# Performance work log

Hardware: AMD Instinct MI355X
Metric: run time of the kernel (lower is better)

## Reference

```python
import jax, jax.numpy as jnp
import numpy as np

EMBED_DIM = 768
NUM_HEADS = 12
HEAD_DIM = EMBED_DIM // NUM_HEADS


def setup_inputs() -> dict:
    key = jax.random.key(0)
    ks = jax.random.split(key, 5)
    B, N, D = 8, 1024, EMBED_DIM
    s = 1.0 / np.sqrt(D)
    x = jax.random.normal(ks[0], (B, N, D), dtype=jnp.float32)
    W_qkv = jax.random.normal(ks[1], (D, 3 * D), dtype=jnp.float32) * s
    b_qkv = jnp.zeros((3 * D,), dtype=jnp.float32)
    W_proj = jax.random.normal(ks[2], (D, D), dtype=jnp.float32) * s
    b_proj = jnp.zeros((D,), dtype=jnp.float32)
    return {"x": x, "W_qkv": W_qkv, "b_qkv": b_qkv, "W_proj": W_proj, "b_proj": b_proj}


def reference(x, W_qkv, b_qkv, W_proj, b_proj):
    B, N, D = x.shape
    H, Hd = NUM_HEADS, HEAD_DIM
    scale = Hd ** -0.5
    qkv = x @ W_qkv + b_qkv                      # (B, N, 3D)
    qkv = qkv.reshape(B, N, 3, H, Hd).transpose(2, 0, 3, 1, 4)  # (3, B, H, N, Hd)
    q, k, v = qkv[0], qkv[1], qkv[2]
    attn = jnp.einsum('bhnd,bhmd->bhnm', q, k) * scale  # (B, H, N, N)
    attn = jax.nn.softmax(attn, axis=-1)
    out = jnp.einsum('bhnm,bhmd->bhnd', attn, v)        # (B, H, N, Hd)
    out = out.transpose(0, 2, 1, 3).reshape(B, N, D)
    return out @ W_proj + b_proj
```

## Files before the change

kernel.cpp:

```cpp
#include <hip/hip_runtime.h>


#define B_   8
#define N_   1024
#define D_   768
#define H_   12
#define HD_  64

typedef __attribute__((ext_vector_type(4))) float f32x4;
typedef __attribute__((ext_vector_type(8))) short bf16x8;

__device__ __forceinline__ unsigned short f2bf(float f) {
    unsigned int u = __float_as_uint(f);
    u += 0x7fff + ((u >> 16) & 1);
    return (unsigned short)(u >> 16);
}
__device__ __forceinline__ unsigned int pk2(float a, float b) {
    return (unsigned int)f2bf(a) | ((unsigned int)f2bf(b) << 16);
}
__device__ __forceinline__ unsigned int pk2t(float a, float b) {
    return __builtin_amdgcn_perm(__float_as_uint(b), __float_as_uint(a), 0x07060302u);
}
__device__ __forceinline__ float truncbf(float f) {
    return __uint_as_float(__float_as_uint(f) & 0xFFFF0000u);
}
__device__ __forceinline__ void gl_lds16(const void* g, void* l) {
    __builtin_amdgcn_global_load_lds(
        (const __attribute__((address_space(1))) unsigned int*)g,
        (__attribute__((address_space(3))) unsigned int*)l, 16, 0, 0);
}
#define MFMA(a, b, c) __builtin_amdgcn_mfma_f32_16x16x32_bf16(a, b, c, 0, 0, 0)
#define BAR() do { __asm__ volatile("" ::: "memory"); \
    __builtin_amdgcn_s_barrier(); \
    __asm__ volatile("" ::: "memory"); } while (0)
#define WAITVM(n) do { __asm__ volatile("" ::: "memory"); \
    __builtin_amdgcn_s_waitcnt(0xF70 | (n)); \
    __asm__ volatile("" ::: "memory"); } while (0)
#define WAITLGKM() __asm__ volatile("s_waitcnt lgkmcnt(0)" ::: "memory")

__global__ __launch_bounds__(256) void prep_kernel(
    const float* __restrict__ x, const float* __restrict__ wqkv,
    const float* __restrict__ wproj,
    unsigned short* __restrict__ XB, unsigned short* __restrict__ WQT,
    unsigned short* __restrict__ WPT)
{
    const int bid = blockIdx.x;
    const int tid = threadIdx.x;
    if (bid < 3072) {
        int id = bid * 256 + tid;
        int r  = id & 127;
        int kc = (id >> 7) & 7;
        int ks = (id >> 10) % 12;
        int nt = id / 12288;
        const float* src = x + (size_t)(nt * 128 + r) * 768 + ks * 64 + kc * 8;
        float4 f0 = *(const float4*)src;
        float4 f1 = *(const float4*)(src + 4);
        uint4 o;
        o.x = pk2(f0.x, f0.y); o.y = pk2(f0.z, f0.w);
        o.z = pk2(f1.x, f1.y); o.w = pk2(f1.z, f1.w);
        *(uint4*)&XB[(size_t)id * 8] = o;
    } else if (bid < 3936) {
        int id = (bid - 3072) * 256 + tid;
        int fr = id & 127;
        int kc = (id >> 7) & 7;
        int ks = (id >> 10) % 12;
        int mt = id / 12288;
        float v[8];
#pragma unroll
        for (int j = 0; j < 8; ++j)
            v[j] = wqkv[(size_t)(ks * 64 + kc * 8 + j) * 2304 + mt * 128 + fr];
        uint4 o;
        o.x = pk2(v[0], v[1]); o.y = pk2(v[2], v[3]);
        o.z = pk2(v[4], v[5]); o.w = pk2(v[6], v[7]);
        *(uint4*)&WQT[(size_t)id * 8] = o;
    } else {
        int id = (bid - 3936) * 256 + tid;
        int fr = id & 63;
        int kc = (id >> 6) & 7;
        int ks = (id >> 9) % 12;
        int nt = id / 6144;
        float v[8];
#pragma unroll
        for (int j = 0; j < 8; ++j)
            v[j] = wproj[(size_t)(ks * 64 + kc * 8 + j) * 768 + nt * 64 + fr];
        uint4 o;
        o.x = pk2(v[0], v[1]); o.y = pk2(v[2], v[3]);
        o.z = pk2(v[4], v[5]); o.w = pk2(v[6], v[7]);
        *(uint4*)&WPT[(size_t)id * 8] = o;
    }
}

__global__ __launch_bounds__(256, 4) void qkv_gemm(
    const unsigned short* __restrict__ XB,
    const unsigned short* __restrict__ WQT,
    const float* __restrict__ bias,
    unsigned short* __restrict__ QS,
    unsigned short* __restrict__ KS,
    unsigned short* __restrict__ VS)
{
    __shared__ __align__(16) unsigned short sm[16384];

    const int tid = threadIdx.x;
    const int w = tid >> 6, lane = tid & 63;
    const int l15 = lane & 15, quad = lane >> 4;
    const int mt = blockIdx.x >> 6;
    const int nt = blockIdx.x & 63;
    const int m0w = (w & 1) * 64, n0w = (w >> 1) * 64;
    const float CS = 0.18033688f;

    char* smb = (char*)sm;
    const char* baseA = (const char*)(WQT + (size_t)(mt * 12) * 8192);
    const char* baseB = (const char*)(XB  + (size_t)(nt * 12) * 8192);

    auto issue = [&](int ks) {
        const char* sA = baseA + ks * 8192;
        const char* sB = baseB + ks * 8192;
        const int pb = ks & 1;
#pragma unroll
        for (int i = 0; i < 2; ++i) {
            const int c = w * 2 + i;
            gl_lds16(sA + (c * 64 + lane) * 16, smb + pb * 8192 + c * 1024);
            gl_lds16(sB + (c * 64 + lane) * 16, smb + 16384 + pb * 8192 + c * 1024);
        }
    };

    f32x4 acc[4][4];
    const f32x4 z = {0.f, 0.f, 0.f, 0.f};
#pragma unroll
    for (int t = 0; t < 4; ++t)
#pragma unroll
        for (int u = 0; u < 4; ++u) acc[t][u] = z;

    issue(0);
    for (int ks = 0; ks < 24; ++ks) {
        BAR();
        if (ks < 23) { issue(ks + 1); WAITVM(4); } else { WAITVM(0); }
        BAR();
        const unsigned short* Ab = sm + (ks & 1) * 4096;
        const unsigned short* Bb = sm + 8192 + (ks & 1) * 4096;
        bf16x8 af[4], bfv[4];
#pragma unroll
        for (int t = 0; t < 4; ++t)
            af[t] = *(const bf16x8*)(Ab + (quad * 128 + m0w + t * 16 + l15) * 8);
#pragma unroll
        for (int u = 0; u < 4; ++u)
            bfv[u] = *(const bf16x8*)(Bb + (quad * 128 + n0w + u * 16 + l15) * 8);
#pragma unroll
        for (int t = 0; t < 4; ++t)
#pragma unroll
            for (int u = 0; u < 4; ++u)
                acc[t][u] = MFMA(af[t], bfv[u], acc[t][u]);
    }

    const int part = mt / 6;
    BAR();

#pragma unroll
    for (int t = 0; t < 4; ++t) {
        int d = m0w + t * 16 + quad * 4;
        float4 bv = *(const float4*)&bias[part * 768 + (mt % 6) * 128 + d];
#pragma unroll
        for (int u = 0; u < 4; ++u) {
            int tok = n0w + u * 16 + l15;
            f32x4 a = acc[t][u];
            float v0 = a[0] + bv.x, v1 = a[1] + bv.y;
            float v2 = a[2] + bv.z, v3 = a[3] + bv.w;
            if (part == 0) { v0 *= CS; v1 *= CS; v2 *= CS; v3 *= CS; }
            if (part < 2) {
                unsigned off = tok * 256 + (((unsigned)(d * 2)) ^ ((tok & 7) << 4));
                uint2 pp; pp.x = pk2(v0, v1); pp.y = pk2(v2, v3);
                *(uint2*)(smb + off) = pp;
            } else {
                float vv[4] = {v0, v1, v2, v3};
#pragma unroll
                for (int r4 = 0; r4 < 4; ++r4) {
                    int dd = d + r4;
                    unsigned off = dd * 256 + (((unsigned)(tok * 2)) ^ ((dd & 7) << 4));
                    *(unsigned short*)(smb + off) = f2bf(vv[r4]);
                }
            }
        }
    }
    BAR();

    const int b = nt >> 3, qtc = nt & 7;
    if (part == 0) {
#pragma unroll
        for (int round = 0; round < 8; ++round) {
            int r = tid & 127;
            int kc = (tid >> 7) + round * 2;
            uint4 val = *(const uint4*)(smb + r * 256 +
                        (((unsigned)(kc << 4)) ^ ((r & 7) << 4)));
            int h = (mt % 6) * 2 + (kc >> 3);
            int bh = b * H_ + h;
            *(uint4*)(QS + (((size_t)(bh * 8 + qtc) * 1024) + (kc & 7) * 128 + r) * 8) = val;
        }
    } else if (part == 1) {
#pragma unroll
        for (int round = 0; round < 8; ++round) {
            int r = tid & 127;
            int kc = (tid >> 7) + round * 2;
            uint4 val = *(const uint4*)(smb + r * 256 +
                        (((unsigned)(kc << 4)) ^ ((r & 7) << 4)));
            int h = (mt % 6) * 2 + (kc >> 3);
            int bh = b * H_ + h;
            int kt = (qtc << 1) | (r >> 6);
            *(uint4*)(KS + (((size_t)(bh * 16 + kt) * 512) + (kc & 7) * 64 + (r & 63)) * 8) = val;
        }
    } else {
#pragma unroll
        for (int round = 0; round < 8; ++round) {
            int dd = tid & 127;
            int tc = (tid >> 7) + round * 2;
            uint4 val = *(const uint4*)(smb + dd * 256 +
                        (((unsigned)(tc << 4)) ^ ((dd & 7) << 4)));
            int h = (mt % 6) * 2 + (dd >> 6);
            int bh = b * H_ + h;
            int kt = (qtc << 1) | (tc >> 3);
            *(uint4*)(VS + (((size_t)(bh * 16 + kt) * 512) + (tc & 7) * 64 + (dd & 63)) * 8) = val;
        }
    }
}

__global__ __launch_bounds__(256, 3) void attn_kernel(
    const unsigned short* __restrict__ QS,
    const unsigned short* __restrict__ KS,
    const unsigned short* __restrict__ VS,
    unsigned short* __restrict__ AWS)
{
    __shared__ __align__(16) unsigned short sm[24576];

    const int tid = threadIdx.x;
    const int w = tid >> 6, lane = tid & 63;
    const int l15 = lane & 15, quad = lane >> 4;
    const int bh = blockIdx.x % 96;
    const int qt = blockIdx.x / 96;

    char* smb = (char*)sm;
    const char* kbase = (const char*)(KS + (size_t)(bh * 16) * 4096);
    const char* vbase = (const char*)(VS + (size_t)(bh * 16) * 4096);

    auto issue_tile = [&](int kt) {
        const char* ks_ = kbase + kt * 8192;
        const char* vs_ = vbase + kt * 8192;
        const int pb = kt & 1;
#pragma unroll
        for (int i = 0; i < 2; ++i) {
            const int c = w * 2 + i;
            gl_lds16(ks_ + (c * 64 + lane) * 16, smb + 16384 + pb * 8192 + c * 1024);
            gl_lds16(vs_ + (c * 64 + lane) * 16, smb + 32768 + pb * 8192 + c * 1024);
        }
    };

    const char* qslab = (const char*)(QS + (size_t)(bh * 8 + qt) * 8192);
#pragma unroll
    for (int i = 0; i < 4; ++i) {
        const int c = w * 4 + i;
        gl_lds16(qslab + (c * 64 + lane) * 16, smb + c * 1024);
    }
    issue_tile(0);

    WAITVM(4);
    BAR();
    bf16x8 qf[2][2];
#pragma unroll
    for (int u = 0; u < 2; ++u)
#pragma unroll
        for (int s = 0; s < 2; ++s)
            qf[u][s] = *(const bf16x8*)(sm + ((s * 4 + quad) * 128 + w * 32 + u * 16 + l15) * 8);
    WAITLGKM();
    BAR();

    f32x4 o[4][2];
    const f32x4 z = {0.f, 0.f, 0.f, 0.f};
#pragma unroll
    for (int t = 0; t < 4; ++t) { o[t][0] = z; o[t][1] = z; }
    float lsum[2] = {0.f, 0.f};

    char* pscr = smb + w * 4096;

    for (int kt = 0; kt < 16; ++kt) {
        BAR();
        if (kt < 15) { issue_tile(kt + 1); WAITVM(4); } else { WAITVM(0); }
        BAR();
        const unsigned short* Kb = sm + 8192 + (kt & 1) * 4096;
        const unsigned short* Vb = sm + 16384 + (kt & 1) * 4096;

        f32x4 s[4][2];
#pragma unroll
        for (int t = 0; t < 4; ++t) { s[t][0] = z; s[t][1] = z; }
#pragma unroll
        for (int ss = 0; ss < 2; ++ss) {
            bf16x8 kf[4];
#pragma unroll
            for (int t = 0; t < 4; ++t)
                kf[t] = *(const bf16x8*)(Kb + ((ss * 4 + quad) * 64 + t * 16 + l15) * 8);
#pragma unroll
            for (int t = 0; t < 4; ++t)
#pragma unroll
                for (int u = 0; u < 2; ++u)
                    s[t][u] = MFMA(kf[t], qf[u][ss], s[t][u]);
        }

#pragma unroll
        for (int u = 0; u < 2; ++u) {
#pragma unroll
            for (int t = 0; t < 4; ++t) {
                float p0 = truncbf(__builtin_amdgcn_exp2f(s[t][u][0]));
                float p1 = truncbf(__builtin_amdgcn_exp2f(s[t][u][1]));
                float p2 = truncbf(__builtin_amdgcn_exp2f(s[t][u][2]));
                float p3 = truncbf(__builtin_amdgcn_exp2f(s[t][u][3]));
                lsum[u] += (p0 + p1) + (p2 + p3);
                uint2 pw; pw.x = pk2t(p0, p1); pw.y = pk2t(p2, p3);
                *(uint2*)(pscr + u * 2048 + l15 * 128 +
                          ((t ^ (l15 & 3)) << 5) + quad * 8) = pw;
            }
        }
        WAITLGKM();

#pragma unroll
        for (int ss = 0; ss < 2; ++ss) {
            bf16x8 vf[4];
#pragma unroll
            for (int t = 0; t < 4; ++t)
                vf[t] = *(const bf16x8*)(Vb + ((ss * 4 + quad) * 64 + t * 16 + l15) * 8);
#pragma unroll
            for (int u = 0; u < 2; ++u) {
                bf16x8 pf = *(const bf16x8*)(pscr + u * 2048 + l15 * 128 +
                            (((2 * ss + (quad >> 1)) ^ (l15 & 3)) << 5) + (quad & 1) * 16);
#pragma unroll
                for (int t = 0; t < 4; ++t)
                    o[t][u] = MFMA(vf[t], pf, o[t][u]);
            }
        }
    }

    float inv[2];
#pragma unroll
    for (int u = 0; u < 2; ++u) {
        float l = lsum[u];
        l += __shfl_xor(l, 16, 64);
        l += __shfl_xor(l, 32, 64);
        inv[u] = 1.f / l;
    }

    BAR();
    char* tb = smb + 16384;
#pragma unroll
    for (int t = 0; t < 4; ++t) {
        int d = t * 16 + quad * 4;
#pragma unroll
        for (int u = 0; u < 2; ++u) {
            int q = w * 32 + u * 16 + l15;
            uint2 pp;
            pp.x = pk2(o[t][u][0] * inv[u], o[t][u][1] * inv[u]);
            pp.y = pk2(o[t][u][2] * inv[u], o[t][u][3] * inv[u]);
            unsigned off = q * 128 + (((unsigned)(d * 2)) ^ ((q & 7) << 4));
            *(uint2*)(tb + off) = pp;
        }
    }
    BAR();
    const int b = bh / H_, h = bh % H_;
    const int mtA = b * 8 + qt;
#pragma unroll
    for (int round = 0; round < 4; ++round) {
        int q = tid & 127;
        int dc = (tid >> 7) + round * 2;
        uint4 val = *(const uint4*)(tb + q * 128 +
                    (((unsigned)(dc << 4)) ^ ((q & 7) << 4)));
        *(uint4*)(AWS + (((size_t)(mtA * 12 + h) * 1024) + dc * 128 + q) * 8) = val;
    }
}

__global__ __launch_bounds__(256, 3) void proj_gemm(
    const unsigned short* __restrict__ AWS,
    const unsigned short* __restrict__ WPT,
    const float* __restrict__ bias, float* __restrict__ out)
{
    __shared__ __align__(16) unsigned short As[2][8192];
    __shared__ __align__(16) unsigned short Bs[2][4096];

    const int tid = threadIdx.x;
    const int w = tid >> 6, lane = tid & 63;
    const int l15 = lane & 15, quad = lane >> 4;
    const int mt = blockIdx.x / 12;
    const int nt = blockIdx.x % 12;
    const int m0w = (w & 1) * 64, n0w = (w >> 1) * 32;

    const char* baseA = (const char*)(AWS + (size_t)(mt * 12) * 8192);
    const char* baseB = (const char*)(WPT + (size_t)(nt * 12) * 4096);

    auto issue = [&](int ks) {
        const char* sA = baseA + ks * 16384;
        const char* sB = baseB + ks * 8192;
        const int pb = ks & 1;
#pragma unroll
        for (int i = 0; i < 4; ++i) {
            const int c = w * 4 + i;
            gl_lds16(sA + (c * 64 + lane) * 16, (char*)As + pb * 16384 + c * 1024);
        }
#pragma unroll
        for (int i = 0; i < 2; ++i) {
            const int c = w * 2 + i;
            gl_lds16(sB + (c * 64 + lane) * 16, (char*)Bs + pb * 8192 + c * 1024);
        }
    };

    f32x4 acc[4][2];
    const f32x4 z = {0.f, 0.f, 0.f, 0.f};
#pragma unroll
    for (int t = 0; t < 4; ++t) { acc[t][0] = z; acc[t][1] = z; }

    issue(0);
    for (int ks = 0; ks < 12; ++ks) {
        BAR();
        if (ks < 11) { issue(ks + 1); WAITVM(6); } else { WAITVM(0); }
        BAR();
        const unsigned short* Ab = As[ks & 1];
        const unsigned short* Bb = Bs[ks & 1];
#pragma unroll
        for (int kk = 0; kk < 2; ++kk) {
            bf16x8 af[4], bfv[2];
#pragma unroll
            for (int t = 0; t < 4; ++t)
                af[t] = *(const bf16x8*)(Ab + (((kk * 4 + quad) * 128) + m0w + t * 16 + l15) * 8);
#pragma unroll
            for (int u = 0; u < 2; ++u)
                bfv[u] = *(const bf16x8*)(Bb + (((kk * 4 + quad) * 64) + n0w + u * 16 + l15) * 8);
#pragma unroll
            for (int t = 0; t < 4; ++t)
#pragma unroll
                for (int u = 0; u < 2; ++u)
                    acc[t][u] = MFMA(af[t], bfv[u], acc[t][u]);
        }
    }

#pragma unroll
    for (int t = 0; t < 4; ++t)
#pragma unroll
        for (int u = 0; u < 2; ++u) {
            int col = nt * 64 + n0w + u * 16 + l15;
            float bvv = bias[col];
#pragma unroll
            for (int r = 0; r < 4; ++r) {
                int row = mt * 128 + m0w + t * 16 + quad * 4 + r;
                out[(size_t)row * 768 + col] = acc[t][u][r] + bvv;
            }
        }
}

extern "C" void kernel_launch(void* const* d_in, const int* in_sizes, int n_in,
                              void* d_out, int out_size, void* d_ws, size_t ws_size,
                              hipStream_t stream) {
    const float* x     = (const float*)d_in[0];
    const float* Wqkv  = (const float*)d_in[1];
    const float* bqkv  = (const float*)d_in[2];
    const float* Wproj = (const float*)d_in[3];
    const float* bproj = (const float*)d_in[4];
    float* out = (float*)d_out;

    unsigned short* ws = (unsigned short*)d_ws;
    unsigned short* XB  = ws;
    unsigned short* WQT = ws + 6291456;
    unsigned short* WPT = ws + 8060928;
    unsigned short* QS  = ws + 8650752;
    unsigned short* KS  = ws + 14942208;
    unsigned short* VS  = ws + 21233664;
    unsigned short* AWS = ws + 27525120;

    prep_kernel<<<dim3(4224), dim3(256), 0, stream>>>(x, Wqkv, Wproj, XB, WQT, WPT);
    qkv_gemm<<<dim3(18 * 64), dim3(256), 0, stream>>>(XB, WQT, bqkv, QS, KS, VS);
    attn_kernel<<<dim3(96 * 8), dim3(256), 0, stream>>>(QS, KS, VS, AWS);
    proj_gemm<<<dim3(64 * 12), dim3(256), 0, stream>>>(AWS, WPT, bproj, out);
}
```

Measured before the change: 184.4 us.

## Switch attention kernel to 32x32x16 MFMA with register-resident P via permlane32 swap

Rewrites the attention inner loop to use 32x32x16 bf16 MFMAs instead of 16x16x32. The softmax probabilities are reshuffled in registers with permlane32_swap, so they no longer pass through an LDS scratch round trip before the PV matmul. The epilogue also writes output directly from registers using permlane swaps, which removes the LDS transpose and its barriers and shrinks shared memory. The exchange is a more intricate lane layout that must match the 32x32 MFMA operand formats, and possibly different register pressure at the same occupancy bound.

```diff
diff --git a/kernel.cpp b/kernel.cpp
--- a/kernel.cpp
+++ b/kernel.cpp
@@ -8,7 +8,10 @@
 #define HD_  64
 
 typedef __attribute__((ext_vector_type(4))) float f32x4;
+typedef __attribute__((ext_vector_type(16))) float f32x16;
 typedef __attribute__((ext_vector_type(8))) short bf16x8;
+typedef __attribute__((ext_vector_type(2))) unsigned int u32x2;
+typedef __attribute__((ext_vector_type(4))) unsigned int u32x4;
 
 __device__ __forceinline__ unsigned short f2bf(float f) {
     unsigned int u = __float_as_uint(f);
@@ -29,7 +32,8 @@
         (const __attribute__((address_space(1))) unsigned int*)g,
         (__attribute__((address_space(3))) unsigned int*)l, 16, 0, 0);
 }
-#define MFMA(a, b, c) __builtin_amdgcn_mfma_f32_16x16x32_bf16(a, b, c, 0, 0, 0)
+#define MFMA(a, b, c)   __builtin_amdgcn_mfma_f32_16x16x32_bf16(a, b, c, 0, 0, 0)
+#define MFMA32(a, b, c) __builtin_amdgcn_mfma_f32_32x32x16_bf16(a, b, c, 0, 0, 0)
 #define BAR() do { __asm__ volatile("" ::: "memory"); \
     __builtin_amdgcn_s_barrier(); \
     __asm__ volatile("" ::: "memory"); } while (0)
@@ -228,11 +232,10 @@
     const unsigned short* __restrict__ VS,
     unsigned short* __restrict__ AWS)
 {
-    __shared__ __align__(16) unsigned short sm[24576];
-
+    __shared__ __align__(16) unsigned short sm[16384];
     const int tid = threadIdx.x;
     const int w = tid >> 6, lane = tid & 63;
-    const int l15 = lane & 15, quad = lane >> 4;
+    const int l31 = lane & 31, h = lane >> 5;
     const int bh = blockIdx.x % 96;
     const int qt = blockIdx.x / 96;
 
@@ -247,8 +250,8 @@
 #pragma unroll
         for (int i = 0; i < 2; ++i) {
             const int c = w * 2 + i;
-            gl_lds16(ks_ + (c * 64 + lane) * 16, smb + 16384 + pb * 8192 + c * 1024);
-            gl_lds16(vs_ + (c * 64 + lane) * 16, smb + 32768 + pb * 8192 + c * 1024);
+            gl_lds16(ks_ + (c * 64 + lane) * 16, smb + pb * 8192 + c * 1024);
+            gl_lds16(vs_ + (c * 64 + lane) * 16, smb + 16384 + pb * 8192 + c * 1024);
         }
     };
 
@@ -256,119 +259,107 @@
 #pragma unroll
     for (int i = 0; i < 4; ++i) {
         const int c = w * 4 + i;
-        gl_lds16(qslab + (c * 64 + lane) * 16, smb + c * 1024);
+        char* dst = (c < 8) ? (smb + 8192 + c * 1024)
+                            : (smb + 24576 + (c - 8) * 1024);
+        gl_lds16(qslab + (c * 64 + lane) * 16, dst);
     }
     issue_tile(0);
 
     WAITVM(4);
     BAR();
-    bf16x8 qf[2][2];
-#pragma unroll
-    for (int u = 0; u < 2; ++u)
-#pragma unroll
-        for (int s = 0; s < 2; ++s)
-            qf[u][s] = *(const bf16x8*)(sm + ((s * 4 + quad) * 128 + w * 32 + u * 16 + l15) * 8);
+    bf16x8 qf[4];
+#pragma unroll
+    for (int ks = 0; ks < 4; ++ks) {
+        const char* qreg = (ks < 2) ? (smb + 8192) : (smb + 24576);
+        const int dcl = (ks & 1) * 2 + h;
+        qf[ks] = *(const bf16x8*)(qreg + (dcl * 128 + w * 32 + l31) * 16);
+    }
     WAITLGKM();
-    BAR();
-
-    f32x4 o[4][2];
-    const f32x4 z = {0.f, 0.f, 0.f, 0.f};
-#pragma unroll
-    for (int t = 0; t < 4; ++t) { o[t][0] = z; o[t][1] = z; }
-    float lsum[2] = {0.f, 0.f};
-
-    char* pscr = smb + w * 4096;
+
+    f32x16 acc[2];
+    const f32x16 z16 = {0.f,0.f,0.f,0.f,0.f,0.f,0.f,0.f,
+                        0.f,0.f,0.f,0.f,0.f,0.f,0.f,0.f};
+    acc[0] = z16; acc[1] = z16;
+    float lsum = 0.f;
 
     for (int kt = 0; kt < 16; ++kt) {
         BAR();
         if (kt < 15) { issue_tile(kt + 1); WAITVM(4); } else { WAITVM(0); }
         BAR();
-        const unsigned short* Kb = sm + 8192 + (kt & 1) * 4096;
-        const unsigned short* Vb = sm + 16384 + (kt & 1) * 4096;
-
-        f32x4 s[4][2];
-#pragma unroll
-        for (int t = 0; t < 4; ++t) { s[t][0] = z; s[t][1] = z; }
-#pragma unroll
-        for (int ss = 0; ss < 2; ++ss) {
-            bf16x8 kf[4];
-#pragma unroll
-            for (int t = 0; t < 4; ++t)
-                kf[t] = *(const bf16x8*)(Kb + ((ss * 4 + quad) * 64 + t * 16 + l15) * 8);
-#pragma unroll
-            for (int t = 0; t < 4; ++t)
-#pragma unroll
-                for (int u = 0; u < 2; ++u)
-                    s[t][u] = MFMA(kf[t], qf[u][ss], s[t][u]);
-        }
-
-#pragma unroll
-        for (int u = 0; u < 2; ++u) {
-#pragma unroll
-            for (int t = 0; t < 4; ++t) {
-                float p0 = truncbf(__builtin_amdgcn_exp2f(s[t][u][0]));
-                float p1 = truncbf(__builtin_amdgcn_exp2f(s[t][u][1]));
-                float p2 = truncbf(__builtin_amdgcn_exp2f(s[t][u][2]));
-                float p3 = truncbf(__builtin_amdgcn_exp2f(s[t][u][3]));
-                lsum[u] += (p0 + p1) + (p2 + p3);
-                uint2 pw; pw.x = pk2t(p0, p1); pw.y = pk2t(p2, p3);
-                *(uint2*)(pscr + u * 2048 + l15 * 128 +
-                          ((t ^ (l15 & 3)) << 5) + quad * 8) = pw;
+        const char* Kb = smb + (kt & 1) * 8192;
+        const char* Vb = smb + 16384 + (kt & 1) * 8192;
+
+        f32x16 sv[2] = {z16, z16};
+#pragma unroll
+        for (int ks = 0; ks < 4; ++ks) {
+#pragma unroll
+            for (int kb = 0; kb < 2; ++kb) {
+                bf16x8 kf = *(const bf16x8*)(Kb +
+                            ((ks * 2 + h) * 64 + kb * 32 + l31) * 16);
+                sv[kb] = MFMA32(kf, qf[ks], sv[kb]);
             }
         }
-        WAITLGKM();
-
-#pragma unroll
-        for (int ss = 0; ss < 2; ++ss) {
-            bf16x8 vf[4];
-#pragma unroll
-            for (int t = 0; t < 4; ++t)
-                vf[t] = *(const bf16x8*)(Vb + ((ss * 4 + quad) * 64 + t * 16 + l15) * 8);
-#pragma unroll
-            for (int u = 0; u < 2; ++u) {
-                bf16x8 pf = *(const bf16x8*)(pscr + u * 2048 + l15 * 128 +
-                            (((2 * ss + (quad >> 1)) ^ (l15 & 3)) << 5) + (quad & 1) * 16);
-#pragma unroll
-                for (int t = 0; t < 4; ++t)
-                    o[t][u] = MFMA(vf[t], pf, o[t][u]);
+
+        unsigned pw[4][4];
+#pragma unroll
+        for (int kb = 0; kb < 2; ++kb) {
+            float p[16];
+#pragma unroll
+            for (int r = 0; r < 16; ++r)
+                p[r] = truncbf(__builtin_amdgcn_exp2f(sv[kb][r]));
+            lsum += ((((p[0] + p[1]) + (p[2] + p[3])) +
+                      ((p[4] + p[5]) + (p[6] + p[7]))) +
+                     (((p[8] + p[9]) + (p[10] + p[11])) +
+                      ((p[12] + p[13]) + (p[14] + p[15]))));
+            unsigned X0 = pk2t(p[0],  p[1]),  X1 = pk2t(p[2],  p[3]);
+            unsigned Y0 = pk2t(p[4],  p[5]),  Y1 = pk2t(p[6],  p[7]);
+            unsigned Z0 = pk2t(p[8],  p[9]),  Z1 = pk2t(p[10], p[11]);
+            unsigned W0 = pk2t(p[12], p[13]), W1 = pk2t(p[14], p[15]);
+            u32x2 a0 = __builtin_amdgcn_permlane32_swap(X0, Y0, false, false);
+            u32x2 a1 = __builtin_amdgcn_permlane32_swap(X1, Y1, false, false);
+            u32x2 b0 = __builtin_amdgcn_permlane32_swap(Z0, W0, false, false);
+            u32x2 b1 = __builtin_amdgcn_permlane32_swap(Z1, W1, false, false);
+            pw[kb * 2][0] = a0[0]; pw[kb * 2][1] = a1[0];
+            pw[kb * 2][2] = a0[1]; pw[kb * 2][3] = a1[1];
+            pw[kb * 2 + 1][0] = b0[0]; pw[kb * 2 + 1][1] = b1[0];
+            pw[kb * 2 + 1][2] = b0[1]; pw[kb * 2 + 1][3] = b1[1];
+        }
+
+#pragma unroll
+        for (int ks = 0; ks < 4; ++ks) {
+            u32x4 pv = {pw[ks][0], pw[ks][1], pw[ks][2], pw[ks][3]};
+            bf16x8 pf = __builtin_bit_cast(bf16x8, pv);
+#pragma unroll
+            for (int db = 0; db < 2; ++db) {
+                bf16x8 vf = *(const bf16x8*)(Vb +
+                            ((ks * 2 + h) * 64 + db * 32 + l31) * 16);
+                acc[db] = MFMA32(vf, pf, acc[db]);
             }
         }
     }
 
-    float inv[2];
-#pragma unroll
-    for (int u = 0; u < 2; ++u) {
-        float l = lsum[u];
-        l += __shfl_xor(l, 16, 64);
-        l += __shfl_xor(l, 32, 64);
-        inv[u] = 1.f / l;
-    }
-
-    BAR();
-    char* tb = smb + 16384;
-#pragma unroll
-    for (int t = 0; t < 4; ++t) {
-        int d = t * 16 + quad * 4;
-#pragma unroll
-        for (int u = 0; u < 2; ++u) {
-            int q = w * 32 + u * 16 + l15;
-            uint2 pp;
-            pp.x = pk2(o[t][u][0] * inv[u], o[t][u][1] * inv[u]);
-            pp.y = pk2(o[t][u][2] * inv[u], o[t][u][3] * inv[u]);
-            unsigned off = q * 128 + (((unsigned)(d * 2)) ^ ((q & 7) << 4));
-            *(uint2*)(tb + off) = pp;
-        }
-    }
-    BAR();
-    const int b = bh / H_, h = bh % H_;
+    float lfull = lsum + __shfl_xor(lsum, 32, 64);
+    float inv = 1.f / lfull;
+
+    const int b = bh / H_, hh = bh % H_;
     const int mtA = b * 8 + qt;
-#pragma unroll
-    for (int round = 0; round < 4; ++round) {
-        int q = tid & 127;
-        int dc = (tid >> 7) + round * 2;
-        uint4 val = *(const uint4*)(tb + q * 128 +
-                    (((unsigned)(dc << 4)) ^ ((q & 7) << 4)));
-        *(uint4*)(AWS + (((size_t)(mtA * 12 + h) * 1024) + dc * 128 + q) * 8) = val;
+    unsigned short* obase = AWS + (size_t)(mtA * 12 + hh) * 8192;
+#pragma unroll
+    for (int db = 0; db < 2; ++db) {
+#pragma unroll
+        for (int gp = 0; gp < 2; ++gp) {
+            const int g0 = gp * 2, g1 = gp * 2 + 1;
+            unsigned v00 = pk2(acc[db][4 * g0 + 0] * inv, acc[db][4 * g0 + 1] * inv);
+            unsigned v01 = pk2(acc[db][4 * g0 + 2] * inv, acc[db][4 * g0 + 3] * inv);
+            unsigned v10 = pk2(acc[db][4 * g1 + 0] * inv, acc[db][4 * g1 + 1] * inv);
+            unsigned v11 = pk2(acc[db][4 * g1 + 2] * inv, acc[db][4 * g1 + 3] * inv);
+            u32x2 t0 = __builtin_amdgcn_permlane32_swap(v00, v10, false, false);
+            u32x2 t1 = __builtin_amdgcn_permlane32_swap(v01, v11, false, false);
+            uint4 val;
+            val.x = t0[0]; val.y = t1[0]; val.z = t0[1]; val.w = t1[1];
+            const int dc = db * 4 + g0 + h;
+            *(uint4*)(obase + ((size_t)(dc * 128) + w * 32 + l31) * 8) = val;
+        }
     }
 }
 
```

After: 180.1 us. 1.02x faster.
